# Kernel tuning notes

Hardware: AMD Instinct MI355X
Metric: run time of the kernel (lower is better)

## Reference

```python
import jax, jax.numpy as jnp
import numpy as np

N, E = 100000, 1600000
IN_C, HID, HEADS, OUT_C = 128, 32, 4, 2
NEG_SLOPE = 0.2


def _gat_layer(x, src, dst, W, a_src, a_dst, b, n_nodes, heads, c):
    # x: [N, F_in] -> h: [N, H, C]
    h = (x @ W).reshape(n_nodes, heads, c)
    alpha_s = jnp.sum(h * a_src, axis=-1)  # [N, H]
    alpha_d = jnp.sum(h * a_dst, axis=-1)  # [N, H]
    e = jax.nn.leaky_relu(alpha_s[src] + alpha_d[dst], NEG_SLOPE)  # [E, H]
    # segment softmax over incoming edges of each dst node
    m = jax.ops.segment_max(e, dst, num_segments=n_nodes)  # [N, H]
    ee = jnp.exp(e - m[dst])
    denom = jax.ops.segment_sum(ee, dst, num_segments=n_nodes)  # [N, H]
    alpha = ee / (denom[dst] + 1e-16)  # [E, H]
    out = jax.ops.segment_sum(h[src] * alpha[:, :, None], dst, num_segments=n_nodes)  # [N, H, C]
    return out.reshape(n_nodes, heads * c) + b


def _gat_forward(x, edge_index, W1, a_src1, a_dst1, b1, W2, a_src2, a_dst2, b2, Wfc, bfc):
    n = x.shape[0]
    loops = jnp.arange(n, dtype=edge_index.dtype)
    src = jnp.concatenate([edge_index[0], loops])  # PyG adds self-loops
    dst = jnp.concatenate([edge_index[1], loops])
    h = jax.nn.elu(_gat_layer(x, src, dst, W1, a_src1, a_dst1, b1, n, HEADS, HID))
    h = jax.nn.elu(_gat_layer(h, src, dst, W2, a_src2, a_dst2, b2, n, HEADS, HID))
    return h @ Wfc + bfc


def setup_inputs() -> dict:
    key = jax.random.key(0)
    ks = jax.random.split(key, 12)
    g = lambda k, shape, fan: jax.random.normal(k, shape, jnp.float32) * (1.0 / np.sqrt(fan))
    return {
        "x": jax.random.normal(ks[0], (N, IN_C), jnp.float32),
        "edge_index": jax.random.randint(ks[1], (2, E), 0, N, jnp.int64),
        "W1": g(ks[2], (IN_C, HEADS * HID), IN_C),
        "a_src1": g(ks[3], (HEADS, HID), HID),
        "a_dst1": g(ks[4], (HEADS, HID), HID),
        "b1": jnp.zeros((HEADS * HID,), jnp.float32),
        "W2": g(ks[5], (HEADS * HID, HEADS * HID), HEADS * HID),
        "a_src2": g(ks[6], (HEADS, HID), HID),
        "a_dst2": g(ks[7], (HEADS, HID), HID),
        "b2": jnp.zeros((HEADS * HID,), jnp.float32),
        "Wfc": g(ks[8], (HEADS * HID, OUT_C), HEADS * HID),
        "bfc": jnp.zeros((OUT_C,), jnp.float32),
    }


def reference(x, edge_index, W1, a_src1, a_dst1, b1, W2, a_src2, a_dst2, b2, Wfc, bfc):
    return _gat_forward(x, edge_index, W1, a_src1, a_dst1, b1, W2, a_src2, a_dst2, b2, Wfc, bfc)
```

## Files before the change

### kernel.cpp

```cpp
#include <hip/hip_runtime.h>
#include <hip/hip_fp16.h>
#include <math.h>

#define FEAT 128
#define NBLK 256
#define BSHIFT 8

typedef _Float16 f16x8 __attribute__((ext_vector_type(8)));
typedef float f32x4 __attribute__((ext_vector_type(4)));

__device__ __forceinline__ float eluf(float x) {
  return x > 0.0f ? x : (__expf(x) - 1.0f);
}


__global__ __launch_bounds__(256) void scan1_kernel(const int* __restrict__ cnt,
                                                    int* __restrict__ pre,
                                                    int* __restrict__ bsum, int n) {
  __shared__ int sd[256];
  const int t = threadIdx.x;
  const int idx = blockIdx.x * 1024 + t * 4;
  int4 v = make_int4(0, 0, 0, 0);
  if (idx + 3 < n) {
    v = *(const int4*)(cnt + idx);
  } else {
    if (idx < n)     v.x = cnt[idx];
    if (idx + 1 < n) v.y = cnt[idx + 1];
    if (idx + 2 < n) v.z = cnt[idx + 2];
    if (idx + 3 < n) v.w = cnt[idx + 3];
  }
  const int tsum = v.x + v.y + v.z + v.w;
  sd[t] = tsum;
  __syncthreads();
  for (int o = 1; o < 256; o <<= 1) {
    int x = (t >= o) ? sd[t - o] : 0;
    __syncthreads();
    sd[t] += x;
    __syncthreads();
  }
  const int excl = sd[t] - tsum;
  if (idx < n)     pre[idx]     = excl;
  if (idx + 1 < n) pre[idx + 1] = excl + v.x;
  if (idx + 2 < n) pre[idx + 2] = excl + v.x + v.y;
  if (idx + 3 < n) pre[idx + 3] = excl + v.x + v.y + v.z;
  if (t == 255) bsum[blockIdx.x] = sd[255];
}

__global__ __launch_bounds__(256) void scan2_kernel(int* __restrict__ bsum, int nb) {
  __shared__ int sd[256];
  const int t = threadIdx.x;
  int v = (t < nb) ? bsum[t] : 0;
  sd[t] = v;
  __syncthreads();
  for (int o = 1; o < 256; o <<= 1) {
    int x = (t >= o) ? sd[t - o] : 0;
    __syncthreads();
    sd[t] += x;
    __syncthreads();
  }
  if (t < nb) bsum[t] = sd[t] - v;
}

__global__ __launch_bounds__(256) void bucket_hist_kernel(
    const int* __restrict__ ei, int* __restrict__ gh,
    int E, int ET, int nbuck, int chunk) {
  __shared__ int h[512];
  const int t = threadIdx.x;
  const int b = blockIdx.x;
  h[t] = 0; h[t + 256] = 0;
  __syncthreads();
  const int lo = b * chunk;
  const int hi = min(lo + chunk, ET);
  for (int i = lo + t; i < hi; i += 256) {
    int d = (i < E) ? ei[E + i] : (i - E);
    atomicAdd(&h[d >> BSHIFT], 1);
  }
  __syncthreads();
  for (int k = t; k < nbuck; k += 256) gh[k * NBLK + b] = h[k];
}

__global__ __launch_bounds__(256) void bucket_scatter_kernel(
    const int* __restrict__ ei, const int* __restrict__ ghp,
    const int* __restrict__ bsum, unsigned* __restrict__ pairs,
    int E, int ET, int nbuck, int chunk) {
  __shared__ int cur[512];
  const int t = threadIdx.x;
  const int b = blockIdx.x;
  for (int k = t; k < nbuck; k += 256) {
    int idx = k * NBLK + b;
    cur[k] = ghp[idx] + bsum[idx >> 10];
  }
  __syncthreads();
  const int lo = b * chunk;
  const int hi = min(lo + chunk, ET);
  for (int i = lo + t; i < hi; i += 256) {
    int s, d;
    if (i < E) { s = ei[i]; d = ei[E + i]; } else { s = d = i - E; }
    int pos = atomicAdd(&cur[d >> BSHIFT], 1);
    pairs[pos] = ((unsigned)s << 8) | (unsigned)(d & 255);
  }
}

__global__ __launch_bounds__(256) void bucket_finalize_kernel(
    const unsigned* __restrict__ pairs, const int* __restrict__ ghp,
    const int* __restrict__ bsum, int* __restrict__ row_ptr,
    int* __restrict__ esrc, int N, int ET, int nbuck) {
  __shared__ int hist[256];
  __shared__ int cur[256];
  __shared__ int sd[256];
  const int t = threadIdx.x;
  const int k = blockIdx.x;
  const int node0 = k << BSHIFT;
  const int idx0 = k * NBLK;
  const int base = ghp[idx0] + bsum[idx0 >> 10];
  int end;
  if (k + 1 < nbuck) {
    const int idx1 = (k + 1) * NBLK;
    end = ghp[idx1] + bsum[idx1 >> 10];
  } else {
    end = ET;
  }
  hist[t] = 0;
  __syncthreads();
  for (int e = base + t; e < end; e += 256) {
    atomicAdd(&hist[pairs[e] & 255u], 1);
  }
  __syncthreads();
  const int v = hist[t];
  __syncthreads();
  sd[t] = v;
  __syncthreads();
  for (int o = 1; o < 256; o <<= 1) {
    int x = (t >= o) ? sd[t - o] : 0;
    __syncthreads();
    sd[t] += x;
    __syncthreads();
  }
  const int excl = sd[t] - v;
  if (node0 + t < N) row_ptr[node0 + t] = base + excl;
  cur[t] = excl;
  __syncthreads();
  for (int e = base + t; e < end; e += 256) {
    unsigned p = pairs[e];
    int pos = atomicAdd(&cur[p & 255u], 1);
    esrc[base + pos] = (int)(p >> 8);
  }
  if (k == 0 && t == 0) row_ptr[N] = ET;
}

__global__ __launch_bounds__(256) void pack_w_kernel(
    const float* __restrict__ W, const float* __restrict__ a_src,
    const float* __restrict__ a_dst, __half* __restrict__ frag) {
  int tid = blockIdx.x * 256 + threadIdx.x;
  if (tid >= 4 * 9 * 64) return;
  int lane = tid & 63;
  int tile = (tid >> 6) % 9;
  int ks = tid / (9 * 64);
  int li = lane & 15, hi = lane >> 4;
  int col = tile * 16 + li;
  __half* dst = frag + (size_t)tid * 8;
  for (int i = 0; i < 8; ++i) {
    int k = ks * 32 + hi * 8 + i;
    float v = 0.f;
    if (col < 128) {
      v = W[k * 128 + col];
    } else if (col < 132) {
      int h = col - 128;
      float s = 0.f;
      for (int j = 0; j < 32; ++j) s += W[k * 128 + h * 32 + j] * a_src[h * 32 + j];
      v = s;
    } else if (col < 136) {
      int h = col - 132;
      float s = 0.f;
      for (int j = 0; j < 32; ++j) s += W[k * 128 + h * 32 + j] * a_dst[h * 32 + j];
      v = s;
    }
    dst[i] = __float2half(v);
  }
}

template <bool F32IN>
__global__ __launch_bounds__(256) void gemm_mfma_kernel(
    const void* __restrict__ in, const __half* __restrict__ frag,
    __half* __restrict__ hout, float* __restrict__ as_out, float* __restrict__ ad_out,
    int nrows) {
  const int wid = (blockIdx.x * 256 + threadIdx.x) >> 6;
  const int lane = threadIdx.x & 63;
  const int li = lane & 15, hi = lane >> 4;
  int row = wid * 16 + li;
  const bool valid = row < nrows;
  if (wid * 16 >= nrows) return;
  if (!valid) row = nrows - 1;

  const f16x8* fragv = (const f16x8*)frag;

  f32x4 acc[9];
#pragma unroll
  for (int t = 0; t < 9; ++t) acc[t] = (f32x4){0.f, 0.f, 0.f, 0.f};

#pragma unroll
  for (int ks = 0; ks < 4; ++ks) {
    f16x8 xf;
    if (F32IN) {
      const float* xp = (const float*)in + (size_t)row * FEAT + ks * 32 + hi * 8;
      float4 v0 = *(const float4*)xp;
      float4 v1 = *(const float4*)(xp + 4);
      xf[0] = (_Float16)v0.x; xf[1] = (_Float16)v0.y;
      xf[2] = (_Float16)v0.z; xf[3] = (_Float16)v0.w;
      xf[4] = (_Float16)v1.x; xf[5] = (_Float16)v1.y;
      xf[6] = (_Float16)v1.z; xf[7] = (_Float16)v1.w;
    } else {
      xf = *(const f16x8*)((const __half*)in + (size_t)row * FEAT + ks * 32 + hi * 8);
    }
#pragma unroll
    for (int t = 0; t < 9; ++t) {
      f16x8 wf = fragv[(ks * 9 + t) * 64 + lane];
      acc[t] = __builtin_amdgcn_mfma_f32_16x16x32_f16(wf, xf, acc[t], 0, 0, 0);
    }
  }

  if (!valid) return;
#pragma unroll
  for (int t = 0; t < 8; ++t) {
    union { __half2 h[2]; uint2 u; } pk;
    pk.h[0] = __floats2half2_rn(acc[t][0], acc[t][1]);
    pk.h[1] = __floats2half2_rn(acc[t][2], acc[t][3]);
    *(uint2*)(hout + (size_t)row * FEAT + t * 16 + hi * 4) = pk.u;
  }
  if (hi == 0) *(float4*)(as_out + row * 4) = make_float4(acc[8][0], acc[8][1], acc[8][2], acc[8][3]);
  if (hi == 1) *(float4*)(ad_out + row * 4) = make_float4(acc[8][0], acc[8][1], acc[8][2], acc[8][3]);
}

template <int MODE>
__global__ __launch_bounds__(256) void node_gat_kernel(
    const int* __restrict__ row_ptr, const int* __restrict__ esrc,
    const float* __restrict__ as_, const float* __restrict__ ad_,
    const __half2* __restrict__ h, const float* __restrict__ bias,
    __half2* __restrict__ out16, const float* __restrict__ fcw,
    const float* __restrict__ fcb, float* __restrict__ outf, int n) {
  const int wid = (blockIdx.x * 256 + threadIdx.x) >> 6;
  if (wid >= n) return;
  const int l = threadIdx.x & 63;
  const int begin = row_ptr[wid];
  const int end = row_ptr[wid + 1];
  const int hd = l >> 4;
  const float adv = ad_[wid * 4 + hd];

  float2 a2 = make_float2(0.f, 0.f);
  float den = 0.f;
  int e = begin;

  for (; e + 7 < end; e += 8) {
    int s[8];
#pragma unroll
    for (int i = 0; i < 8; ++i) s[i] = esrc[e + i];
    float as8[8];
#pragma unroll
    for (int i = 0; i < 8; ++i) as8[i] = as_[s[i] * 4 + hd];
    float2 hv[8];
#pragma unroll
    for (int i = 0; i < 8; ++i) hv[i] = __half22float2(h[(size_t)s[i] * 64 + l]);
#pragma unroll
    for (int i = 0; i < 8; ++i) {
      const float x = as8[i] + adv;
      const float w = __expf(fmaxf(x, 0.2f * x));
      den += w;
      a2.x = fmaf(hv[i].x, w, a2.x);
      a2.y = fmaf(hv[i].y, w, a2.y);
    }
  }
  for (; e + 3 < end; e += 4) {
    int s[4];
#pragma unroll
    for (int i = 0; i < 4; ++i) s[i] = esrc[e + i];
    float as4[4];
#pragma unroll
    for (int i = 0; i < 4; ++i) as4[i] = as_[s[i] * 4 + hd];
    float2 hv[4];
#pragma unroll
    for (int i = 0; i < 4; ++i) hv[i] = __half22float2(h[(size_t)s[i] * 64 + l]);
#pragma unroll
    for (int i = 0; i < 4; ++i) {
      const float x = as4[i] + adv;
      const float w = __expf(fmaxf(x, 0.2f * x));
      den += w;
      a2.x = fmaf(hv[i].x, w, a2.x);
      a2.y = fmaf(hv[i].y, w, a2.y);
    }
  }
  for (; e < end; ++e) {
    const int s0 = esrc[e];
    const float x = as_[s0 * 4 + hd] + adv;
    const float w = __expf(fmaxf(x, 0.2f * x));
    const float2 h0 = __half22float2(h[(size_t)s0 * 64 + l]);
    den += w;
    a2.x = fmaf(h0.x, w, a2.x);
    a2.y = fmaf(h0.y, w, a2.y);
  }

  const float inv = 1.0f / (den + 1e-16f);
  const float o0 = a2.x * inv;
  const float o1 = a2.y * inv;
  const float2 b = *(const float2*)(bias + l * 2);
  if (MODE == 0) {
    out16[(size_t)wid * 64 + l] = __floats2half2_rn(eluf(o0 + b.x), eluf(o1 + b.y));
  } else {
    const float e0 = eluf(o0 + b.x);
    const float e1 = eluf(o1 + b.y);
    const float4 w4 = *(const float4*)(fcw + l * 4);
    float s0 = e0 * w4.x + e1 * w4.z;
    float s1 = e0 * w4.y + e1 * w4.w;
#pragma unroll
    for (int o = 32; o >= 1; o >>= 1) {
      s0 += __shfl_xor(s0, o);
      s1 += __shfl_xor(s1, o);
    }
    if (l == 0) {
      *(float2*)(outf + (size_t)wid * 2) = make_float2(s0 + fcb[0], s1 + fcb[1]);
    }
  }
}

extern "C" void kernel_launch(void* const* d_in, const int* in_sizes, int n_in,
                              void* d_out, int out_size, void* d_ws, size_t ws_size,
                              hipStream_t stream) {
  const float* x   = (const float*)d_in[0];
  const int*   ei  = (const int*)d_in[1];
  const float* W1  = (const float*)d_in[2];
  const float* as1 = (const float*)d_in[3];
  const float* ad1 = (const float*)d_in[4];
  const float* b1  = (const float*)d_in[5];
  const float* W2  = (const float*)d_in[6];
  const float* as2 = (const float*)d_in[7];
  const float* ad2 = (const float*)d_in[8];
  const float* b2  = (const float*)d_in[9];
  const float* Wfc = (const float*)d_in[10];
  const float* bfc = (const float*)d_in[11];
  float* out = (float*)d_out;

  const int N = in_sizes[0] / FEAT;
  const int E = in_sizes[1] / 2;
  const int ET = E + N;
  const int nbuck = (N + 255) >> BSHIFT;
  const int NN = nbuck * NBLK;
  const int chunk = (ET + NBLK - 1) / NBLK;

  char* ws = (char*)d_ws;
  __half* hraw = (__half*)ws;
  __half* hin2 = hraw + (size_t)N * FEAT;
  float* acc   = (float*)(hin2 + (size_t)N * FEAT);
  float* asb   = acc + (size_t)N * FEAT;
  float* adb   = asb + (size_t)N * 4;
  __half* bfrag1 = (__half*)(adb + (size_t)N * 4);
  __half* bfrag2 = bfrag1 + 4 * 9 * 64 * 8;
  int* bsum    = (int*)(bfrag2 + 4 * 9 * 64 * 8);
  int* row_ptr = bsum + 256;
  int* esrc    = row_ptr + (N + 1);
  int* gh    = (int*)acc;
  int* ghp   = gh + NN;
  unsigned* pairs = (unsigned*)(ghp + NN);

  const dim3 b256(256);
  const int nb = (NN + 1023) / 1024;

  pack_w_kernel<<<9, b256, 0, stream>>>(W1, as1, ad1, bfrag1);
  pack_w_kernel<<<9, b256, 0, stream>>>(W2, as2, ad2, bfrag2);

  bucket_hist_kernel<<<NBLK, b256, 0, stream>>>(ei, gh, E, ET, nbuck, chunk);
  scan1_kernel<<<nb, b256, 0, stream>>>(gh, ghp, bsum, NN);
  scan2_kernel<<<1, b256, 0, stream>>>(bsum, nb);
  bucket_scatter_kernel<<<NBLK, b256, 0, stream>>>(ei, ghp, bsum, pairs, E, ET, nbuck, chunk);
  bucket_finalize_kernel<<<nbuck, b256, 0, stream>>>(pairs, ghp, bsum, row_ptr, esrc, N, ET, nbuck);

  const int ntiles = (N + 15) / 16;
  const int ggrid = (ntiles + 3) / 4;
  const int wgrid = (N * 64 + 255) / 256;

  gemm_mfma_kernel<true><<<ggrid, b256, 0, stream>>>(x, bfrag1, hraw, asb, adb, N);
  node_gat_kernel<0><<<wgrid, b256, 0, stream>>>(row_ptr, esrc, asb, adb,
                                                 (const __half2*)hraw, b1,
                                                 (__half2*)hin2, nullptr, nullptr, nullptr, N);

  gemm_mfma_kernel<false><<<ggrid, b256, 0, stream>>>(hin2, bfrag2, hraw, asb, adb, N);
  node_gat_kernel<1><<<wgrid, b256, 0, stream>>>(row_ptr, esrc, asb, adb,
                                                 (const __half2*)hraw, b2,
                                                 nullptr, Wfc, bfc, out, N);
}
```

Baseline: 268.5 us.

## Cooperatively load edge indices and compute attention weights once per lane

The per-node aggregation now processes edges in chunks of 16. Each lane loads one edge source index and computes one exp weight per head, then broadcasts indices with readlane and weights with ds_bpermute. Previously every lane redundantly loaded all source indices and alpha values and evaluated exp for every edge. This cuts redundant scalar loads and transcendental work, at the cost of cross-lane permute traffic and a 16-edge chunk granularity with a masked remainder path.

```diff
diff --git a/kernel.cpp b/kernel.cpp
--- a/kernel.cpp
+++ b/kernel.cpp
@@ -241,61 +241,58 @@
   const int wid = (blockIdx.x * 256 + threadIdx.x) >> 6;
   if (wid >= n) return;
   const int l = threadIdx.x & 63;
+  const int j = l & 15;
+  const int g = l >> 4;
   const int begin = row_ptr[wid];
   const int end = row_ptr[wid + 1];
-  const int hd = l >> 4;
-  const float adv = ad_[wid * 4 + hd];
+  const float adv = ad_[wid * 4 + g];
+  const int hdbase = g * 64;
 
   float2 a2 = make_float2(0.f, 0.f);
   float den = 0.f;
+
   int e = begin;
-
-  for (; e + 7 < end; e += 8) {
-    int s[8];
-#pragma unroll
-    for (int i = 0; i < 8; ++i) s[i] = esrc[e + i];
-    float as8[8];
-#pragma unroll
-    for (int i = 0; i < 8; ++i) as8[i] = as_[s[i] * 4 + hd];
-    float2 hv[8];
-#pragma unroll
-    for (int i = 0; i < 8; ++i) hv[i] = __half22float2(h[(size_t)s[i] * 64 + l]);
-#pragma unroll
-    for (int i = 0; i < 8; ++i) {
-      const float x = as8[i] + adv;
-      const float w = __expf(fmaxf(x, 0.2f * x));
-      den += w;
-      a2.x = fmaf(hv[i].x, w, a2.x);
-      a2.y = fmaf(hv[i].y, w, a2.y);
-    }
-  }
-  for (; e + 3 < end; e += 4) {
-    int s[4];
-#pragma unroll
-    for (int i = 0; i < 4; ++i) s[i] = esrc[e + i];
-    float as4[4];
-#pragma unroll
-    for (int i = 0; i < 4; ++i) as4[i] = as_[s[i] * 4 + hd];
-    float2 hv[4];
-#pragma unroll
-    for (int i = 0; i < 4; ++i) hv[i] = __half22float2(h[(size_t)s[i] * 64 + l]);
-#pragma unroll
-    for (int i = 0; i < 4; ++i) {
-      const float x = as4[i] + adv;
-      const float w = __expf(fmaxf(x, 0.2f * x));
-      den += w;
-      a2.x = fmaf(hv[i].x, w, a2.x);
-      a2.y = fmaf(hv[i].y, w, a2.y);
-    }
-  }
-  for (; e < end; ++e) {
-    const int s0 = esrc[e];
-    const float x = as_[s0 * 4 + hd] + adv;
+  for (; e + 16 <= end; e += 16) {
+    const int s = esrc[e + j];
+    const float x = as_[s * 4 + g] + adv;
     const float w = __expf(fmaxf(x, 0.2f * x));
-    const float2 h0 = __half22float2(h[(size_t)s0 * 64 + l]);
-    den += w;
-    a2.x = fmaf(h0.x, w, a2.x);
-    a2.y = fmaf(h0.y, w, a2.y);
+    __half2 hv[16];
+#pragma unroll
+    for (int k = 0; k < 16; ++k) {
+      const int sk = __builtin_amdgcn_readlane(s, k);
+      hv[k] = h[(size_t)(unsigned)sk * 64 + l];
+    }
+#pragma unroll
+    for (int k = 0; k < 16; ++k) {
+      const float wk = __int_as_float(
+          __builtin_amdgcn_ds_bpermute(hdbase + 4 * k, __float_as_int(w)));
+      den += wk;
+      a2.x = fmaf((float)hv[k].x, wk, a2.x);
+      a2.y = fmaf((float)hv[k].y, wk, a2.y);
+    }
+  }
+  const int rem = end - e;
+  if (rem > 0) {
+    const int idx = e + (j < rem ? j : rem - 1);
+    const int s = esrc[idx];
+    const float x = as_[s * 4 + g] + adv;
+    const float w = __expf(fmaxf(x, 0.2f * x));
+    __half2 hv[16];
+#pragma unroll
+    for (int k = 0; k < 16; ++k) {
+      if (k >= rem) break;
+      const int sk = __builtin_amdgcn_readlane(s, k);
+      hv[k] = h[(size_t)(unsigned)sk * 64 + l];
+    }
+#pragma unroll
+    for (int k = 0; k < 16; ++k) {
+      if (k >= rem) break;
+      const float wk = __int_as_float(
+          __builtin_amdgcn_ds_bpermute(hdbase + 4 * k, __float_as_int(w)));
+      den += wk;
+      a2.x = fmaf((float)hv[k].x, wk, a2.x);
+      a2.y = fmaf((float)hv[k].y, wk, a2.y);
+    }
   }
 
   const float inv = 1.0f / (den + 1e-16f);
```

Measured after the change: 345.3 us. 1.29x slower.
